# Optimization experiments

Hardware: AMD Instinct MI355X
Metric: run time of the kernel (lower is better)

## Reference

```python
import jax, jax.numpy as jnp
import numpy as np

N_NODES = 8192
N_EDGES = 65536
NB = 10            # number_of_basis
MID = 32           # middle_layer_size
MAX_R = 10.0       # max_radius
NZ, NM = 48, 16    # z / mol embedding sizes -> 64x0e node input
IN_S = NZ + NM     # 64 scalars
H_S, H_V = 32, 8   # hidden irreps 32x0e + 8x1o (dim 56)
O_S = 16           # output irreps 16x0e
W0N = IN_S * H_S + IN_S * H_V                                  # 2560
W1N = H_S*H_S + H_V*H_S + H_S*H_V + H_V*H_V + H_V*H_V          # 1664
W2N = H_S*O_S + H_V*O_S                                        # 640
H_DIM = H_S + 3 * H_V                                          # 56


def _fcnet(e, W1, W2):
    # e3nn FullyConnectedNet([NB, MID, numel], silu): fan-in normalized linears
    h = jax.nn.silu(e @ W1 / np.sqrt(W1.shape[0]))
    return h @ W2 / np.sqrt(W2.shape[0])


def _ln(x, g, b):
    m = jnp.mean(x, -1, keepdims=True)
    v = jnp.var(x, -1, keepdims=True)
    return (x - m) * jax.lax.rsqrt(v + 1e-5) * g + b


def _sus(t):
    # smooth compact-support bump helper: exp(-1/t) for t>0 else 0
    return jnp.where(t > 0, jnp.exp(-1.0 / jnp.where(t > 0, t, 1.0)), 0.0)


def _forward(pos, Ez, Em,
             b0_W1, b0_W2, b0_g, b0_b,
             b1_W1, b1_W2, b1_g, b1_b,
             b2_W1, b2_W2, b2_g, b2_b,
             z, mol_id, edge_src, edge_dst):
    N = pos.shape[0]
    E = edge_src.shape[0]
    avg = E / N  # avg_num_neighbors (static)

    # node embedding: 64x0e
    x = jnp.concatenate([Ez[z], Em[mol_id]], axis=-1)          # [N, 64]

    vec = pos[edge_dst] - pos[edge_src]                        # [E, 3]
    length = jnp.linalg.norm(vec, axis=1)                      # [E]

    # soft_one_hot_linspace(basis='smooth_finite', cutoff=True) * sqrt(NB)
    vals = jnp.linspace(0.0, MAX_R, NB + 2)[1:-1]
    step = MAX_R / (NB + 1)
    u = (length[:, None] - vals) / step
    emb = (1.14136 * np.exp(2.0)) * _sus(u + 1.0) * _sus(1.0 - u)
    emb = emb * np.sqrt(NB)                                    # [E, NB]

    # spherical harmonics lmax=1, normalize=True, 'component' norm
    nrm = vec / jnp.maximum(length, 1e-9)[:, None]
    sh_v = np.sqrt(3.0) * nrm                                  # [E, 3]  (l=1; l=0 comp == 1)

    # ---- interaction block 0: 64x0e -> 32x0e + 8x1o ----
    w = _fcnet(emb, b0_W1, b0_W2)                              # [E, 2560]
    w00 = w[:, :IN_S * H_S].reshape(E, IN_S, H_S)
    w01 = w[:, IN_S * H_S:].reshape(E, IN_S, H_V)
    xe = x[edge_src]                                           # [E, 64]
    es = jnp.einsum('eu,euw->ew', xe, w00) / np.sqrt(IN_S)
    ev = jnp.einsum('eu,euw,ei->ewi', xe, w01, sh_v) / np.sqrt(IN_S)
    msg = jnp.concatenate([es, ev.reshape(E, 3 * H_V)], -1)    # [E, 56]
    x = _ln(jax.ops.segment_sum(msg, edge_dst, num_segments=N) / np.sqrt(avg), b0_g, b0_b)

    # ---- interaction block 1: 32x0e+8x1o -> 32x0e+8x1o ----
    w = _fcnet(emb, b1_W1, b1_W2)                              # [E, 1664]
    o = 0
    w_ss  = w[:, o:o + H_S*H_S].reshape(E, H_S, H_S); o += H_S*H_S
    w_vvs = w[:, o:o + H_V*H_S].reshape(E, H_V, H_S); o += H_V*H_S
    w_sv  = w[:, o:o + H_S*H_V].reshape(E, H_S, H_V); o += H_S*H_V
    w_vs  = w[:, o:o + H_V*H_V].reshape(E, H_V, H_V); o += H_V*H_V
    w_vvv = w[:, o:o + H_V*H_V].reshape(E, H_V, H_V)
    xs = x[:, :H_S][edge_src]                                  # [E, 32]
    xv = x[:, H_S:].reshape(N, H_V, 3)[edge_src]               # [E, 8, 3]
    dot = jnp.einsum('eui,ei->eu', xv, sh_v) / np.sqrt(3.0)    # 1o x 1o -> 0e CG
    crs = jnp.cross(xv, sh_v[:, None, :]) / np.sqrt(2.0)       # 1o x 1o -> 1o CG
    es = (jnp.einsum('eu,euw->ew', xs, w_ss) / np.sqrt(H_S)
          + jnp.einsum('eu,euw->ew', dot, w_vvs) / np.sqrt(H_V)) / np.sqrt(2.0)
    ev = (jnp.einsum('eu,euw,ei->ewi', xs, w_sv, sh_v) / np.sqrt(H_S)
          + jnp.einsum('eui,euw->ewi', xv, w_vs) / np.sqrt(H_V)
          + jnp.einsum('eui,euw->ewi', crs, w_vvv) / np.sqrt(H_V)) / np.sqrt(3.0)
    msg = jnp.concatenate([es, ev.reshape(E, 3 * H_V)], -1)
    x = _ln(jax.ops.segment_sum(msg, edge_dst, num_segments=N) / np.sqrt(avg), b1_g, b1_b)

    # ---- interaction block 2: 32x0e+8x1o -> 16x0e ----
    w = _fcnet(emb, b2_W1, b2_W2)                              # [E, 640]
    w_ss  = w[:, :H_S * O_S].reshape(E, H_S, O_S)
    w_vvs = w[:, H_S * O_S:].reshape(E, H_V, O_S)
    xs = x[:, :H_S][edge_src]
    xv = x[:, H_S:].reshape(N, H_V, 3)[edge_src]
    dot = jnp.einsum('eui,ei->eu', xv, sh_v) / np.sqrt(3.0)
    es = (jnp.einsum('eu,euw->ew', xs, w_ss) / np.sqrt(H_S)
          + jnp.einsum('eu,euw->ew', dot, w_vvs) / np.sqrt(H_V)) / np.sqrt(2.0)
    x = _ln(jax.ops.segment_sum(es, edge_dst, num_segments=N) / np.sqrt(avg), b2_g, b2_b)
    return x                                                   # [N, 16]


def setup_inputs():
    key = jax.random.key(0)
    ks = jax.random.split(key, 16)
    edge_src = jax.random.randint(ks[3], (N_EDGES,), 0, N_NODES)
    # exclude self-loops (radius_graph never returns them)
    edge_dst = (edge_src + 1 + jax.random.randint(ks[4], (N_EDGES,), 0, N_NODES - 1)) % N_NODES
    return {
        'pos': jax.random.uniform(ks[0], (N_NODES, 3), jnp.float32) * 8.0,
        'z': jax.random.randint(ks[1], (N_NODES,), 0, 100),
        'mol_id': jax.random.randint(ks[2], (N_NODES,), 0, 2),
        'edge_src': edge_src,
        'edge_dst': edge_dst,
        'Ez': jax.random.normal(ks[5], (100, NZ), jnp.float32),
        'Em': jax.random.normal(ks[6], (2, NM), jnp.float32),
        'b0_W1': jax.random.normal(ks[7], (NB, MID), jnp.float32),
        'b0_W2': jax.random.normal(ks[8], (MID, W0N), jnp.float32),
        'b0_g': jnp.ones((H_DIM,), jnp.float32),
        'b0_b': jnp.zeros((H_DIM,), jnp.float32),
        'b1_W1': jax.random.normal(ks[9], (NB, MID), jnp.float32),
        'b1_W2': jax.random.normal(ks[10], (MID, W1N), jnp.float32),
        'b1_g': jnp.ones((H_DIM,), jnp.float32),
        'b1_b': jnp.zeros((H_DIM,), jnp.float32),
        'b2_W1': jax.random.normal(ks[11], (NB, MID), jnp.float32),
        'b2_W2': jax.random.normal(ks[12], (MID, W2N), jnp.float32),
        'b2_g': jnp.ones((O_S,), jnp.float32),
        'b2_b': jnp.zeros((O_S,), jnp.float32),
    }


def reference(pos, z, mol_id, edge_src, edge_dst, Ez, Em,
              b0_W1, b0_W2, b0_g, b0_b,
              b1_W1, b1_W2, b1_g, b1_b,
              b2_W1, b2_W2, b2_g, b2_b):
    return _forward(pos, Ez, Em,
                    b0_W1, b0_W2, b0_g, b0_b,
                    b1_W1, b1_W2, b1_g, b1_b,
                    b2_W1, b2_W2, b2_g, b2_b,
                    z, mol_id, edge_src, edge_dst)
```

## Files before the change

kernel.cpp:

```cpp
#include <hip/hip_runtime.h>

#define NNODES 8192
#define NEDGES 65536

#define K_PACK   0.02209708691f
#define K_P1SV   0.01804219593f
#define K_VVS    0.04419417382f
#define K_VS     0.03608439182f
#define K_VVV    0.02551551815f
#define K_DOT    0.57735026919f
#define K_PRELN  0.35355339059f
#define C_EMB    8.4335730689f

typedef unsigned int uint32;
typedef unsigned short ushort16;
typedef __attribute__((ext_vector_type(8))) short short8;
typedef __attribute__((ext_vector_type(4))) float floatx4;

__device__ __forceinline__ float siluf(float x) { return x / (1.0f + __expf(-x)); }
__device__ __forceinline__ float susf(float t) { return t > 0.0f ? __expf(-1.0f / t) : 0.0f; }
__device__ __forceinline__ ushort16 f2bf(float f) {
  uint32 u = __float_as_uint(f);
  return (ushort16)((u + 0x7fffu + ((u >> 16) & 1u)) >> 16);
}
__device__ __forceinline__ float bflo(uint32 v) { return __uint_as_float(v << 16); }
__device__ __forceinline__ float bfhi(uint32 v) { return __uint_as_float(v & 0xffff0000u); }
__device__ __forceinline__ float bfs(ushort16 v) { return __uint_as_float((uint32)v << 16); }

__global__ __launch_bounds__(256) void k_prep(
    const float* __restrict__ pos, const int* __restrict__ z, const int* __restrict__ mol,
    const int* __restrict__ esrc, const int* __restrict__ edst,
    const float* __restrict__ Ez, const float* __restrict__ Em,
    const float* __restrict__ W10, const float* __restrict__ W11, const float* __restrict__ W12,
    const float* __restrict__ W20, const float* __restrict__ W21, const float* __restrict__ W22,
    int* __restrict__ combo, ushort16* __restrict__ X0cb, float* __restrict__ sh,
    ushort16* __restrict__ h0b, ushort16* __restrict__ h1b, ushort16* __restrict__ h2b,
    ushort16* __restrict__ Bp0, ushort16* __restrict__ Bp1, ushort16* __restrict__ Bp2,
    ushort16* __restrict__ Bpw1, ushort16* __restrict__ Bpw2,
    int* __restrict__ deg, int* __restrict__ eidx) {
  __shared__ float Wl[320];
  int b = blockIdx.x;
  if (b < 768) {
    int which = b >> 8;
    int e = ((b & 255) << 8) + threadIdx.x;
    const float* W = (which == 0) ? W10 : (which == 1) ? W11 : W12;
    for (int i = threadIdx.x; i < 320; i += 256) Wl[i] = W[i];
    __syncthreads();
    int s = esrc[e], d = edst[e];
    float vx = pos[d * 3 + 0] - pos[s * 3 + 0];
    float vy = pos[d * 3 + 1] - pos[s * 3 + 1];
    float vz = pos[d * 3 + 2] - pos[s * 3 + 2];
    float len = sqrtf(vx * vx + vy * vy + vz * vz);
    if (which == 0) {
      int p = atomicAdd(&deg[d], 1);
      if (p < 64) eidx[(size_t)d * 64 + p] = e;
      float inv = 1.7320508076f / fmaxf(len, 1e-9f);
      sh[e * 3 + 0] = vx * inv; sh[e * 3 + 1] = vy * inv; sh[e * 3 + 2] = vz * inv;
    }
    float emb[10];
#pragma unroll
    for (int k = 0; k < 10; ++k) {
      float u = len * 1.1f - (float)(k + 1);
      emb[k] = C_EMB * susf(u + 1.0f) * susf(1.0f - u);
    }
    float H[32];
#pragma unroll
    for (int m = 0; m < 32; ++m) {
      float t = 0.f;
#pragma unroll
      for (int k = 0; k < 10; ++k) t += emb[k] * Wl[k * 32 + m];
      H[m] = siluf(t);
    }
    ushort16* hb = (which == 0) ? h0b : (which == 1) ? h1b : h2b;
    uint32* hp = (uint32*)(hb + (size_t)e * 32);
#pragma unroll
    for (int m = 0; m < 16; ++m)
      hp[m] = (uint32)f2bf(H[2 * m]) | ((uint32)f2bf(H[2 * m + 1]) << 16);
    return;
  }
  int idx = (b - 768) * 256 + threadIdx.x;
  if (idx < NNODES) { combo[idx] = z[idx] * 2 + mol[idx]; return; }
  idx -= NNODES;
  if (idx < 16384) {
    int c = idx >> 6, j = idx & 63;
    float v = 0.f;
    if (c < 200) {
      int zz = c >> 1, mm = c & 1;
      v = (j < 48) ? Ez[zz * 48 + j] : Em[mm * 16 + (j - 48)];
    }
    X0cb[idx] = f2bf(v);
    return;
  }
  idx -= 16384;
  if (idx < 81920) {
    int tile = idx >> 10; int r = idx & 1023;
    int kh = r >> 9; int rr = r & 511;
    int lane = rr >> 3, j = rr & 7;
    int k = kh * 32 + (lane >> 4) * 8 + j;
    int n = tile * 16 + (lane & 15);
    int c = n >> 5, m = n & 31;
    int col = (c < 32) ? (k * 32 + c) : (2048 + k * 8 + (c - 32));
    Bp0[idx] = f2bf(W20[m * 2560 + col] * K_PACK);
    return;
  }
  idx -= 81920;
  if (idx < 40960) {
    int tile = idx >> 9; int rr = idx & 511;
    int lane = rr >> 3, j = rr & 7;
    int k = (lane >> 4) * 8 + j;
    int n = tile * 16 + (lane & 15);
    int c = n >> 5, m = n & 31;
    float v = (c < 32) ? W21[m * 1664 + k * 32 + c] * K_PACK
                       : W21[m * 1664 + 1280 + k * 8 + (c - 32)] * K_P1SV;
    Bp1[idx] = f2bf(v);
    return;
  }
  idx -= 40960;
  if (idx < 16384) {
    int tile = idx >> 9; int rr = idx & 511;
    int lane = rr >> 3, j = rr & 7;
    int k = (lane >> 4) * 8 + j;
    int n = tile * 16 + (lane & 15);
    int c = n >> 5, m = n & 31;
    Bp2[idx] = f2bf(W22[m * 640 + k * 16 + c] * K_PACK);
    return;
  }
  idx -= 16384;
  if (idx < 12288) {
    int tile = idx >> 9; int rr = idx & 511;
    int lane = rr >> 3, j = rr & 7;
    int m = (lane >> 4) * 8 + j;
    int n = tile * 16 + (lane & 15);
    float v;
    if (n < 256) {
      int c = n >> 3, u = n & 7;
      v = W21[m * 1664 + 1024 + u * 32 + c] * K_VVS;
    } else if (n < 320) {
      int vo = (n - 256) >> 3, u = n & 7;
      v = W21[m * 1664 + 1536 + u * 8 + vo] * K_VS;
    } else {
      int vo = (n - 320) >> 3, u = n & 7;
      v = W21[m * 1664 + 1600 + u * 8 + vo] * K_VVV;
    }
    Bpw1[idx] = f2bf(v);
    return;
  }
  idx -= 12288;
  {
    int tile = idx >> 9; int rr = idx & 511;
    int lane = rr >> 3, j = rr & 7;
    int m = (lane >> 4) * 8 + j;
    int n = tile * 16 + (lane & 15);
    int c = n >> 3, u = n & 7;
    Bpw2[idx] = f2bf(W22[m * 640 + 512 + u * 16 + c] * K_VVS);
  }
}

__device__ __forceinline__ void gemm_tile(
    const ushort16* __restrict__ A, const ushort16* __restrict__ Bp, ushort16* __restrict__ C,
    int N, int K, int bx, int by, int wave, int lane) {
  int m0 = bx * 64 + wave * 16;
  int n0 = by * 64;
  int row = lane & 15, q = lane >> 4;
  int nkh = K >> 5;
  floatx4 acc[4];
  floatx4 zero = {0.f, 0.f, 0.f, 0.f};
#pragma unroll
  for (int t = 0; t < 4; ++t) acc[t] = zero;
  for (int kh = 0; kh < nkh; ++kh) {
    short8 a = *reinterpret_cast<const short8*>(A + (size_t)(m0 + row) * K + kh * 32 + q * 8);
#pragma unroll
    for (int t = 0; t < 4; ++t) {
      int T = (n0 >> 4) + t;
      short8 b = *reinterpret_cast<const short8*>(Bp + ((size_t)T * nkh + kh) * 512 + lane * 8);
      acc[t] = __builtin_amdgcn_mfma_f32_16x16x32_bf16(a, b, acc[t], 0, 0, 0);
    }
  }
  int colb = n0 + row;
#pragma unroll
  for (int t = 0; t < 4; ++t)
#pragma unroll
    for (int r = 0; r < 4; ++r)
      C[(size_t)(m0 + q * 4 + r) * N + colb + t * 16] = f2bf(acc[t][r]);
}

__global__ __launch_bounds__(256) void k_gemm_mfma(
    const ushort16* __restrict__ A, const ushort16* __restrict__ Bp, ushort16* __restrict__ C,
    int N, int K) {
  gemm_tile(A, Bp, C, N, K, blockIdx.x, blockIdx.y, threadIdx.x >> 6, threadIdx.x & 63);
}

__global__ __launch_bounds__(256) void k_msg0(
    const int* __restrict__ rowmap, const int* __restrict__ esrc,
    const float* __restrict__ sh, const ushort16* __restrict__ hb,
    const ushort16* __restrict__ Pb, ushort16* __restrict__ msg) {
  __shared__ float pdl[4][48];
  int w = threadIdx.x >> 6;
  int e = __builtin_amdgcn_readfirstlane(blockIdx.x * 4 + w);
  int lane = threadIdx.x & 63;
  int row = lane & 15, q = lane >> 4;
  int s = esrc[e];
  int rp = __builtin_amdgcn_readfirstlane(rowmap[s]);
  float sh0 = sh[e * 3 + 0], sh1 = sh[e * 3 + 1], sh2 = sh[e * 3 + 2];
  int c; float mult;
  if (lane < 32) { c = lane; mult = 1.0f; }
  else if (lane < 56) {
    int l = lane - 32; int v = l / 3; int i = l - v * 3;
    c = 32 + v;
    mult = (i == 0) ? sh0 : (i == 1 ? sh1 : sh2);
  } else { c = 0; mult = 0.0f; }
  short8 af = *reinterpret_cast<const short8*>(hb + (size_t)e * 32 + q * 8);
  int c2 = 32 + row; if (c2 > 39) c2 = 39;
  const ushort16* Pr = Pb + (size_t)rp * 1280;
  short8 bf0 = *reinterpret_cast<const short8*>(Pr + row * 32 + q * 8);
  short8 bf1 = *reinterpret_cast<const short8*>(Pr + (16 + row) * 32 + q * 8);
  short8 bf2 = *reinterpret_cast<const short8*>(Pr + c2 * 32 + q * 8);
  floatx4 pz = {0.f, 0.f, 0.f, 0.f};
  floatx4 p0 = __builtin_amdgcn_mfma_f32_16x16x32_bf16(af, bf0, pz, 0, 0, 0);
  floatx4 p1 = __builtin_amdgcn_mfma_f32_16x16x32_bf16(af, bf1, pz, 0, 0, 0);
  floatx4 p2 = __builtin_amdgcn_mfma_f32_16x16x32_bf16(af, bf2, pz, 0, 0, 0);
  if (lane < 16) {
    pdl[w][lane] = p0[0];
    pdl[w][16 + lane] = p1[0];
    if (lane < 8) pdl[w][32 + lane] = p2[0];
  }
  float pdot = pdl[w][c];
  if (lane < 56) msg[(size_t)e * 56 + lane] = f2bf(pdot * mult);
}

__global__ __launch_bounds__(256) void k_msg1f(
    const int* __restrict__ esrc, const float* __restrict__ sh, const ushort16* __restrict__ hb,
    const ushort16* __restrict__ Pb, const float* __restrict__ xv,
    const ushort16* __restrict__ Bpw, ushort16* __restrict__ msg) {
  __shared__ ushort16 Wlds[16][392];
  __shared__ float pdl[4][48];
  int w = threadIdx.x >> 6, lane = threadIdx.x & 63;
  int e0 = __builtin_amdgcn_readfirstlane(blockIdx.x * 16);
  int row = lane & 15, q = lane >> 4;
  short8 a1 = *reinterpret_cast<const short8*>(hb + (size_t)(e0 + row) * 32 + q * 8);
  floatx4 zero = {0.f, 0.f, 0.f, 0.f};
#pragma unroll
  for (int t6 = 0; t6 < 6; ++t6) {
    int T = w * 6 + t6;
    short8 b1 = *reinterpret_cast<const short8*>(Bpw + (size_t)T * 512 + lane * 8);
    floatx4 acc = __builtin_amdgcn_mfma_f32_16x16x32_bf16(a1, b1, zero, 0, 0, 0);
#pragma unroll
    for (int r = 0; r < 4; ++r)
      Wlds[q * 4 + r][T * 16 + row] = f2bf(acc[r]);
  }
  __syncthreads();
  int lv = lane - 32;
  int vq = (lv >= 0) ? ((lv / 3 > 7) ? 7 : lv / 3) : 0;
  int vi = (lv >= 0) ? (lv - (lv / 3) * 3) : 0;
  int c = (lane < 32) ? lane : 32 + vq;
  int c2 = 32 + row; if (c2 > 39) c2 = 39;
#pragma unroll
  for (int k = 0; k < 4; ++k) {
    int e = e0 + w * 4 + k;
    int s = __builtin_amdgcn_readfirstlane(esrc[e]);
    float sh0 = sh[e * 3 + 0], sh1 = sh[e * 3 + 1], sh2 = sh[e * 3 + 2];
    const float* xr = xv + (size_t)s * 24;
    const ushort16* wp = &Wlds[w * 4 + k][0];
    float vterm, mult;
    if (lane < 32) {
      mult = 1.0f;
      uint4 wv = *reinterpret_cast<const uint4*>(wp + lane * 8);
      float ww[8] = {bflo(wv.x), bfhi(wv.x), bflo(wv.y), bfhi(wv.y),
                     bflo(wv.z), bfhi(wv.z), bflo(wv.w), bfhi(wv.w)};
      vterm = 0.f;
#pragma unroll
      for (int u = 0; u < 8; ++u) {
        float du = K_DOT * (xr[u * 3] * sh0 + xr[u * 3 + 1] * sh1 + xr[u * 3 + 2] * sh2);
        vterm += du * ww[u];
      }
    } else {
      float shi = (vi == 0) ? sh0 : (vi == 1) ? sh1 : sh2;
      float s1 = (vi == 0) ? sh1 : (vi == 1) ? sh2 : sh0;
      float s2 = (vi == 0) ? sh2 : (vi == 1) ? sh0 : sh1;
      mult = shi;
      uint4 wvs = *reinterpret_cast<const uint4*>(wp + 256 + vq * 8);
      uint4 wvv = *reinterpret_cast<const uint4*>(wp + 320 + vq * 8);
      float vsw[8] = {bflo(wvs.x), bfhi(wvs.x), bflo(wvs.y), bfhi(wvs.y),
                      bflo(wvs.z), bfhi(wvs.z), bflo(wvs.w), bfhi(wvs.w)};
      float vvw[8] = {bflo(wvv.x), bfhi(wvv.x), bflo(wvv.y), bfhi(wvv.y),
                      bflo(wvv.z), bfhi(wvv.z), bflo(wvv.w), bfhi(wvv.w)};
      vterm = 0.f;
#pragma unroll
      for (int u = 0; u < 8; ++u) {
        float xu0 = xr[u * 3], xu1 = xr[u * 3 + 1], xu2 = xr[u * 3 + 2];
        float xui = (vi == 0) ? xu0 : (vi == 1) ? xu1 : xu2;
        float xi1 = (vi == 0) ? xu1 : (vi == 1) ? xu2 : xu0;
        float xi2 = (vi == 0) ? xu2 : (vi == 1) ? xu0 : xu1;
        float crs = xi1 * s2 - xi2 * s1;
        vterm += xui * vsw[u] + crs * vvw[u];
      }
    }
    short8 af = *reinterpret_cast<const short8*>(hb + (size_t)e * 32 + q * 8);
    const ushort16* Pr = Pb + (size_t)s * 1280;
    short8 bf0 = *reinterpret_cast<const short8*>(Pr + row * 32 + q * 8);
    short8 bf1 = *reinterpret_cast<const short8*>(Pr + (16 + row) * 32 + q * 8);
    short8 bf2 = *reinterpret_cast<const short8*>(Pr + c2 * 32 + q * 8);
    floatx4 p0 = __builtin_amdgcn_mfma_f32_16x16x32_bf16(af, bf0, zero, 0, 0, 0);
    floatx4 p1 = __builtin_amdgcn_mfma_f32_16x16x32_bf16(af, bf1, zero, 0, 0, 0);
    floatx4 p2 = __builtin_amdgcn_mfma_f32_16x16x32_bf16(af, bf2, zero, 0, 0, 0);
    if (lane < 16) {
      pdl[w][lane] = p0[0];
      pdl[w][16 + lane] = p1[0];
      if (lane < 8) pdl[w][32 + lane] = p2[0];
    }
    float pdot = pdl[w][c];
    if (lane < 56) msg[(size_t)e * 56 + lane] = f2bf(pdot * mult + vterm);
  }
}

__global__ __launch_bounds__(256) void k_msg2f(
    const int* __restrict__ esrc, const float* __restrict__ sh, const ushort16* __restrict__ hb,
    const ushort16* __restrict__ Pb, const float* __restrict__ xv,
    const ushort16* __restrict__ Bpw, ushort16* __restrict__ msg) {
  __shared__ ushort16 Wlds[16][136];
  int w = threadIdx.x >> 6, lane = threadIdx.x & 63;
  int e0 = __builtin_amdgcn_readfirstlane(blockIdx.x * 16);
  int row = lane & 15, q = lane >> 4;
  short8 a1 = *reinterpret_cast<const short8*>(hb + (size_t)(e0 + row) * 32 + q * 8);
  floatx4 zero = {0.f, 0.f, 0.f, 0.f};
#pragma unroll
  for (int t2 = 0; t2 < 2; ++t2) {
    int T = w * 2 + t2;
    short8 b1 = *reinterpret_cast<const short8*>(Bpw + (size_t)T * 512 + lane * 8);
    floatx4 acc = __builtin_amdgcn_mfma_f32_16x16x32_bf16(a1, b1, zero, 0, 0, 0);
#pragma unroll
    for (int r = 0; r < 4; ++r)
      Wlds[q * 4 + r][T * 16 + row] = f2bf(acc[r]);
  }
  __syncthreads();
  int cch = lane & 15;
#pragma unroll
  for (int k = 0; k < 4; ++k) {
    int e = e0 + w * 4 + k;
    int s = __builtin_amdgcn_readfirstlane(esrc[e]);
    float sh0 = sh[e * 3 + 0], sh1 = sh[e * 3 + 1], sh2 = sh[e * 3 + 2];
    const float* xr = xv + (size_t)s * 24;
    uint4 wv = *reinterpret_cast<const uint4*>(&Wlds[w * 4 + k][0] + cch * 8);
    float ww[8] = {bflo(wv.x), bfhi(wv.x), bflo(wv.y), bfhi(wv.y),
                   bflo(wv.z), bfhi(wv.z), bflo(wv.w), bfhi(wv.w)};
    float vterm = 0.f;
#pragma unroll
    for (int u = 0; u < 8; ++u) {
      float du = K_DOT * (xr[u * 3] * sh0 + xr[u * 3 + 1] * sh1 + xr[u * 3 + 2] * sh2);
      vterm += du * ww[u];
    }
    short8 af = *reinterpret_cast<const short8*>(hb + (size_t)e * 32 + q * 8);
    short8 bf = *reinterpret_cast<const short8*>(Pb + (size_t)s * 512 + row * 32 + q * 8);
    floatx4 p0 = __builtin_amdgcn_mfma_f32_16x16x32_bf16(af, bf, zero, 0, 0, 0);
    if (lane < 16) msg[(size_t)e * 16 + lane] = f2bf(p0[0] + vterm);
  }
}

__global__ __launch_bounds__(256) void k_gather_ln(
    const int* __restrict__ deg, const int* __restrict__ eidx,
    const ushort16* __restrict__ msg, int D,
    const float* __restrict__ g, const float* __restrict__ b,
    ushort16* __restrict__ xsb, float* __restrict__ xvf, float* __restrict__ outf) {
  int n = __builtin_amdgcn_readfirstlane(blockIdx.x * 4 + (threadIdx.x >> 6));
  int lane = threadIdx.x & 63;
  int cnt = deg[n]; if (cnt > 64) cnt = 64;
  const int* ep = eidx + (size_t)n * 64;
  float v = 0.f;
  for (int j = 0; j < cnt; ++j) {
    int e = ep[j];
    if (lane < D) v += bfs(msg[(size_t)e * D + lane]);
  }
  v *= K_PRELN;
  if (lane >= D) v = 0.f;
  float sm = v, sq = v * v;
#pragma unroll
  for (int off = 32; off > 0; off >>= 1) {
    sm += __shfl_xor(sm, off, 64);
    sq += __shfl_xor(sq, off, 64);
  }
  float invD = 1.0f / (float)D;
  float mean = sm * invD;
  float var = sq * invD - mean * mean;
  float rs = rsqrtf(var + 1e-5f);
  float r = (v - mean) * rs * g[lane < D ? lane : 0] + b[lane < D ? lane : 0];
  if (outf) {
    if (lane < D) outf[(size_t)n * D + lane] = r;
  } else {
    if (lane < 32) xsb[(size_t)n * 32 + lane] = f2bf(r);
    else if (lane < 56) xvf[(size_t)n * 24 + lane - 32] = r;
  }
}

extern "C" void kernel_launch(void* const* d_in, const int* in_sizes, int n_in,
                              void* d_out, int out_size, void* d_ws, size_t ws_size,
                              hipStream_t stream) {
  const float* pos = (const float*)d_in[0];
  const int* z = (const int*)d_in[1];
  const int* mol = (const int*)d_in[2];
  const int* esrc = (const int*)d_in[3];
  const int* edst = (const int*)d_in[4];
  const float* Ez = (const float*)d_in[5];
  const float* Em = (const float*)d_in[6];
  const float* b0W1 = (const float*)d_in[7];
  const float* b0W2 = (const float*)d_in[8];
  const float* b0g = (const float*)d_in[9];
  const float* b0b = (const float*)d_in[10];
  const float* b1W1 = (const float*)d_in[11];
  const float* b1W2 = (const float*)d_in[12];
  const float* b1g = (const float*)d_in[13];
  const float* b1b = (const float*)d_in[14];
  const float* b2W1 = (const float*)d_in[15];
  const float* b2W2 = (const float*)d_in[16];
  const float* b2g = (const float*)d_in[17];
  const float* b2b = (const float*)d_in[18];
  float* out = (float*)d_out;

  float* ws = (float*)d_ws;
  size_t o = 0;
  int* combo = (int*)(ws + o); o += NNODES;
  int* deg = (int*)(ws + o); o += NNODES;
  int* eidx = (int*)(ws + o); o += (size_t)NNODES * 64;
  ushort16* X0cb = (ushort16*)(ws + o); o += 8192;
  ushort16* xs1b = (ushort16*)(ws + o); o += 131072;
  float* xv1 = ws + o; o += (size_t)NNODES * 24;
  ushort16* h0b = (ushort16*)(ws + o); o += (size_t)NEDGES * 16;
  ushort16* h1b = (ushort16*)(ws + o); o += (size_t)NEDGES * 16;
  ushort16* h2b = (ushort16*)(ws + o); o += (size_t)NEDGES * 16;
  float* shb = ws + o; o += (size_t)NEDGES * 3;
  ushort16* Bp0 = (ushort16*)(ws + o); o += 40960;
  ushort16* Bp1 = (ushort16*)(ws + o); o += 20480;
  ushort16* Bp2 = (ushort16*)(ws + o); o += 8192;
  ushort16* Bpw1 = (ushort16*)(ws + o); o += 6144;
  ushort16* Bpw2 = (ushort16*)(ws + o); o += 2048;
  ushort16* P12 = (ushort16*)(ws + o); o += (size_t)NNODES * 640;
  ushort16* msgb = (ushort16*)(ws + o); o += (size_t)NEDGES * 28;

  ushort16* P0c = P12;
  ushort16* xs2b = xs1b;
  float* xv2 = xv1;
  ushort16* msg16 = msgb;

  hipMemsetAsync(deg, 0, NNODES * sizeof(int), stream);

  k_prep<<<1472, 256, 0, stream>>>(pos, z, mol, esrc, edst, Ez, Em,
                                   b0W1, b1W1, b2W1, b0W2, b1W2, b2W2,
                                   combo, X0cb, shb, h0b, h1b, h2b,
                                   Bp0, Bp1, Bp2, Bpw1, Bpw2, deg, eidx);

  k_gemm_mfma<<<dim3(4, 20), 256, 0, stream>>>(X0cb, Bp0, P0c, 1280, 64);
  k_msg0<<<16384, 256, 0, stream>>>(combo, esrc, shb, h0b, P0c, msgb);
  k_gather_ln<<<2048, 256, 0, stream>>>(deg, eidx, msgb, 56, b0g, b0b, xs1b, xv1, nullptr);

  k_gemm_mfma<<<dim3(128, 20), 256, 0, stream>>>(xs1b, Bp1, P12, 1280, 32);
  k_msg1f<<<4096, 256, 0, stream>>>(esrc, shb, h1b, P12, xv1, Bpw1, msgb);
  k_gather_ln<<<2048, 256, 0, stream>>>(deg, eidx, msgb, 56, b1g, b1b, xs2b, xv2, nullptr);

  k_gemm_mfma<<<dim3(128, 8), 256, 0, stream>>>(xs2b, Bp2, P12, 512, 32);
  k_msg2f<<<4096, 256, 0, stream>>>(esrc, shb, h2b, P12, xv2, Bpw2, msg16);
  k_gather_ln<<<2048, 256, 0, stream>>>(deg, eidx, msg16, 16, b2g, b2b, nullptr, nullptr, out);
}
```

Measured before the change: 215.7 us.

## Fuse block-0 message computation into destination-node gather with layernorm

Replaces the per-edge k_msg0 kernel and the following gather/layernorm with one destination-centric kernel. Each wave walks a node's incoming edges, computes the messages with MFMA and accumulates them in registers before applying the layernorm. This removes the write and re-read of the edge message buffer for block 0 and one kernel launch. The loop runs serially over up to 64 edges per wave, so latency depends on the degree distribution. The LDS exchange of MFMA results in msg0/msg1f is also replaced with a cross-lane shuffle.

```diff
diff --git a/kernel.cpp b/kernel.cpp
--- a/kernel.cpp
+++ b/kernel.cpp
@@ -190,42 +190,57 @@
   gemm_tile(A, Bp, C, N, K, blockIdx.x, blockIdx.y, threadIdx.x >> 6, threadIdx.x & 63);
 }
 
-__global__ __launch_bounds__(256) void k_msg0(
-    const int* __restrict__ rowmap, const int* __restrict__ esrc,
+__global__ __launch_bounds__(256) void k_gather0(
+    const int* __restrict__ deg, const int* __restrict__ eidx,
+    const int* __restrict__ combo, const int* __restrict__ esrc,
     const float* __restrict__ sh, const ushort16* __restrict__ hb,
-    const ushort16* __restrict__ Pb, ushort16* __restrict__ msg) {
-  __shared__ float pdl[4][48];
-  int w = threadIdx.x >> 6;
-  int e = __builtin_amdgcn_readfirstlane(blockIdx.x * 4 + w);
+    const ushort16* __restrict__ Pb,
+    const float* __restrict__ g, const float* __restrict__ b,
+    ushort16* __restrict__ xsb, float* __restrict__ xvf) {
+  int n = __builtin_amdgcn_readfirstlane(blockIdx.x * 4 + (threadIdx.x >> 6));
   int lane = threadIdx.x & 63;
   int row = lane & 15, q = lane >> 4;
-  int s = esrc[e];
-  int rp = __builtin_amdgcn_readfirstlane(rowmap[s]);
-  float sh0 = sh[e * 3 + 0], sh1 = sh[e * 3 + 1], sh2 = sh[e * 3 + 2];
-  int c; float mult;
-  if (lane < 32) { c = lane; mult = 1.0f; }
-  else if (lane < 56) {
-    int l = lane - 32; int v = l / 3; int i = l - v * 3;
-    c = 32 + v;
-    mult = (i == 0) ? sh0 : (i == 1 ? sh1 : sh2);
-  } else { c = 0; mult = 0.0f; }
-  short8 af = *reinterpret_cast<const short8*>(hb + (size_t)e * 32 + q * 8);
+  int cnt = deg[n]; if (cnt > 64) cnt = 64;
+  const int* ep = eidx + (size_t)n * 64;
+  int lv = lane - 32;
+  int vq = (lv >= 0) ? ((lv / 3 > 7) ? 7 : lv / 3) : 0;
+  int vi = (lv >= 0) ? (lv - (lv / 3) * 3) : 0;
   int c2 = 32 + row; if (c2 > 39) c2 = 39;
-  const ushort16* Pr = Pb + (size_t)rp * 1280;
-  short8 bf0 = *reinterpret_cast<const short8*>(Pr + row * 32 + q * 8);
-  short8 bf1 = *reinterpret_cast<const short8*>(Pr + (16 + row) * 32 + q * 8);
-  short8 bf2 = *reinterpret_cast<const short8*>(Pr + c2 * 32 + q * 8);
-  floatx4 pz = {0.f, 0.f, 0.f, 0.f};
-  floatx4 p0 = __builtin_amdgcn_mfma_f32_16x16x32_bf16(af, bf0, pz, 0, 0, 0);
-  floatx4 p1 = __builtin_amdgcn_mfma_f32_16x16x32_bf16(af, bf1, pz, 0, 0, 0);
-  floatx4 p2 = __builtin_amdgcn_mfma_f32_16x16x32_bf16(af, bf2, pz, 0, 0, 0);
-  if (lane < 16) {
-    pdl[w][lane] = p0[0];
-    pdl[w][16 + lane] = p1[0];
-    if (lane < 8) pdl[w][32 + lane] = p2[0];
-  }
-  float pdot = pdl[w][c];
-  if (lane < 56) msg[(size_t)e * 56 + lane] = f2bf(pdot * mult);
+  floatx4 zero = {0.f, 0.f, 0.f, 0.f};
+  float v = 0.f;
+  for (int j = 0; j < cnt; ++j) {
+    int e = __builtin_amdgcn_readfirstlane(ep[j]);
+    int s = __builtin_amdgcn_readfirstlane(esrc[e]);
+    int rp = __builtin_amdgcn_readfirstlane(combo[s]);
+    float sh0 = sh[e * 3 + 0], sh1 = sh[e * 3 + 1], sh2 = sh[e * 3 + 2];
+    short8 af = *reinterpret_cast<const short8*>(hb + (size_t)e * 32 + q * 8);
+    const ushort16* Pr = Pb + (size_t)rp * 1280;
+    short8 bf0 = *reinterpret_cast<const short8*>(Pr + row * 32 + q * 8);
+    short8 bf1 = *reinterpret_cast<const short8*>(Pr + (16 + row) * 32 + q * 8);
+    short8 bf2 = *reinterpret_cast<const short8*>(Pr + c2 * 32 + q * 8);
+    floatx4 p0 = __builtin_amdgcn_mfma_f32_16x16x32_bf16(af, bf0, zero, 0, 0, 0);
+    floatx4 p1 = __builtin_amdgcn_mfma_f32_16x16x32_bf16(af, bf1, zero, 0, 0, 0);
+    floatx4 p2 = __builtin_amdgcn_mfma_f32_16x16x32_bf16(af, bf2, zero, 0, 0, 0);
+    float pv2 = __shfl(p2[0], vq, 64);
+    float pdot = (lane < 16) ? p0[0] : (lane < 32) ? p1[0] : pv2;
+    float mult = (lane < 32) ? 1.0f : ((vi == 0) ? sh0 : (vi == 1) ? sh1 : sh2);
+    v += pdot * mult;
+  }
+  v *= K_PRELN;
+  if (lane >= 56) v = 0.f;
+  float sm = v, sq = v * v;
+#pragma unroll
+  for (int off = 32; off > 0; off >>= 1) {
+    sm += __shfl_xor(sm, off, 64);
+    sq += __shfl_xor(sq, off, 64);
+  }
+  float invD = 1.0f / 56.0f;
+  float mean = sm * invD;
+  float var = sq * invD - mean * mean;
+  float rs = rsqrtf(var + 1e-5f);
+  float r = (v - mean) * rs * g[lane < 56 ? lane : 0] + b[lane < 56 ? lane : 0];
+  if (lane < 32) xsb[(size_t)n * 32 + lane] = f2bf(r);
+  else if (lane < 56) xvf[(size_t)n * 24 + lane - 32] = r;
 }
 
 __global__ __launch_bounds__(256) void k_msg1f(
@@ -233,7 +248,6 @@
     const ushort16* __restrict__ Pb, const float* __restrict__ xv,
     const ushort16* __restrict__ Bpw, ushort16* __restrict__ msg) {
   __shared__ ushort16 Wlds[16][392];
-  __shared__ float pdl[4][48];
   int w = threadIdx.x >> 6, lane = threadIdx.x & 63;
   int e0 = __builtin_amdgcn_readfirstlane(blockIdx.x * 16);
   int row = lane & 15, q = lane >> 4;
@@ -252,7 +266,6 @@
   int lv = lane - 32;
   int vq = (lv >= 0) ? ((lv / 3 > 7) ? 7 : lv / 3) : 0;
   int vi = (lv >= 0) ? (lv - (lv / 3) * 3) : 0;
-  int c = (lane < 32) ? lane : 32 + vq;
   int c2 = 32 + row; if (c2 > 39) c2 = 39;
 #pragma unroll
   for (int k = 0; k < 4; ++k) {
@@ -303,12 +316,8 @@
     floatx4 p0 = __builtin_amdgcn_mfma_f32_16x16x32_bf16(af, bf0, zero, 0, 0, 0);
     floatx4 p1 = __builtin_amdgcn_mfma_f32_16x16x32_bf16(af, bf1, zero, 0, 0, 0);
     floatx4 p2 = __builtin_amdgcn_mfma_f32_16x16x32_bf16(af, bf2, zero, 0, 0, 0);
-    if (lane < 16) {
-      pdl[w][lane] = p0[0];
-      pdl[w][16 + lane] = p1[0];
-      if (lane < 8) pdl[w][32 + lane] = p2[0];
-    }
-    float pdot = pdl[w][c];
+    float pv2 = __shfl(p2[0], vq, 64);
+    float pdot = (lane < 16) ? p0[0] : (lane < 32) ? p1[0] : pv2;
     if (lane < 56) msg[(size_t)e * 56 + lane] = f2bf(pdot * mult + vterm);
   }
 }
@@ -448,8 +457,8 @@
                                    Bp0, Bp1, Bp2, Bpw1, Bpw2, deg, eidx);
 
   k_gemm_mfma<<<dim3(4, 20), 256, 0, stream>>>(X0cb, Bp0, P0c, 1280, 64);
-  k_msg0<<<16384, 256, 0, stream>>>(combo, esrc, shb, h0b, P0c, msgb);
-  k_gather_ln<<<2048, 256, 0, stream>>>(deg, eidx, msgb, 56, b0g, b0b, xs1b, xv1, nullptr);
+  k_gather0<<<2048, 256, 0, stream>>>(deg, eidx, combo, esrc, shb, h0b, P0c,
+                                      b0g, b0b, xs1b, xv1);
 
   k_gemm_mfma<<<dim3(128, 20), 256, 0, stream>>>(xs1b, Bp1, P12, 1280, 32);
   k_msg1f<<<4096, 256, 0, stream>>>(esrc, shb, h1b, P12, xv1, Bpw1, msgb);
```

Result: faster. 205.3 us (-4.8%).
